# Optimization experiments

Hardware: AMD Instinct MI355X
Metric: run time of the kernel (lower is better)

## Reference

```python
import jax, jax.numpy as jnp
import numpy as np

EPS = 1e-6

def layernorm(x, alpha, bias):
    # torch.std default is unbiased (ddof=1)
    mean = x.mean(axis=-1, keepdims=True)
    std = jnp.std(x, axis=-1, keepdims=True, ddof=1)
    return alpha * (x - mean) / (std + EPS) + bias


def setup_inputs() -> dict:
    key = jax.random.key(0)
    B, L, d_model = 2, 1024, 1024
    d_state, d_conv, expand = 16, 4, 2
    d_inner = expand * d_model
    ks = jax.random.split(key, 8)
    std = 0.02
    x = jax.random.normal(ks[0], (B, L, d_model), dtype=jnp.float32)
    in_proj_w = jax.random.normal(ks[1], (2 * d_inner, d_model), dtype=jnp.float32) * std
    in_proj_b = jnp.zeros((2 * d_inner,), jnp.float32)
    conv_w = jax.random.normal(ks[2], (d_inner, 1, d_conv), dtype=jnp.float32) * std  # depthwise, groups=d_inner
    conv_b = jnp.zeros((d_inner,), jnp.float32)
    x_proj_w = jax.random.normal(ks[3], (2 * d_state, d_inner), dtype=jnp.float32) * std
    x_proj_b = jnp.zeros((2 * d_state,), jnp.float32)
    dt_proj_w = jax.random.normal(ks[4], (d_inner, d_inner), dtype=jnp.float32) * std
    dt_proj_b = jnp.zeros((d_inner,), jnp.float32)
    A_log = jnp.log(jnp.tile(jnp.arange(1, d_state + 1, dtype=jnp.float32), (d_inner, 1)))
    D = jnp.ones((d_inner,), jnp.float32)
    out_proj_w = jax.random.normal(ks[5], (d_model, d_inner), dtype=jnp.float32) * std
    out_proj_b = jnp.zeros((d_model,), jnp.float32)
    in_norm_alpha = jnp.ones((d_model,), jnp.float32)
    in_norm_bias = jnp.zeros((d_model,), jnp.float32)
    norm_alpha = jnp.ones((d_model,), jnp.float32)
    norm_bias = jnp.zeros((d_model,), jnp.float32)
    return {"x": x, "in_proj_w": in_proj_w, "in_proj_b": in_proj_b,
            "conv_w": conv_w, "conv_b": conv_b,
            "x_proj_w": x_proj_w, "x_proj_b": x_proj_b,
            "dt_proj_w": dt_proj_w, "dt_proj_b": dt_proj_b,
            "A_log": A_log, "D": D,
            "out_proj_w": out_proj_w, "out_proj_b": out_proj_b,
            "in_norm_alpha": in_norm_alpha, "in_norm_bias": in_norm_bias,
            "norm_alpha": norm_alpha, "norm_bias": norm_bias}


def reference(x, in_proj_w, in_proj_b, conv_w, conv_b, x_proj_w, x_proj_b,
              dt_proj_w, dt_proj_b, A_log, D, out_proj_w, out_proj_b,
              in_norm_alpha, in_norm_bias, norm_alpha, norm_bias):
    batch, L, d_model = x.shape
    d_inner = D.shape[0]
    d_state = A_log.shape[1]
    d_conv = conv_w.shape[-1]

    residual = x
    xn = layernorm(x, in_norm_alpha, in_norm_bias)
    xz = xn @ in_proj_w.T + in_proj_b                    # (B, L, 2*d_inner)
    x_in, z = jnp.split(xz, 2, axis=-1)

    # causal depthwise conv: torch pads both sides by d_conv-1 then slices [:L]
    # -> equivalent to left-pad only
    xc = jnp.swapaxes(x_in, 1, 2)                        # (B, d_inner, L)
    xc = jax.lax.conv_general_dilated(
        xc, conv_w, window_strides=(1,), padding=[(d_conv - 1, 0)],
        dimension_numbers=('NCH', 'OIH', 'NCH'),
        feature_group_count=d_inner) + conv_b[None, :, None]
    xc = jax.nn.silu(jnp.swapaxes(xc, 1, 2))             # (B, L, d_inner)

    Bmat, Cmat = jnp.split(xc @ x_proj_w.T + x_proj_b, 2, axis=-1)  # (B, L, d_state) each
    delta = jnp.clip(jax.nn.softplus(xc @ dt_proj_w.T + dt_proj_b), 1e-4, 10.0)
    A = -jnp.exp(A_log)                                  # (d_inner, d_state)
    flags = (jnp.arange(L) % 16) == 15                   # periodic renorm mask

    def step(h, inp):
        d_t, B_t, C_t, x_t, flag = inp                   # d_t,x_t: (B,d_inner); B_t,C_t: (B,d_state)
        dA = jnp.exp(jnp.clip(d_t[..., None] * A, -10.0, 0.0))      # (B,d_inner,d_state)
        dBx = d_t[..., None] * B_t[:, None, :] * x_t[..., None]
        h = dA * h + dBx
        hn = jnp.maximum(jnp.linalg.norm(h, axis=-1, keepdims=True), 1e-6)
        scale = jnp.where(hn > 10.0, 10.0 / hn, 1.0)
        h = jnp.where(flag, h * scale, h)
        y_t = jnp.sum(C_t[:, None, :] * h, axis=-1) + D * x_t
        return h, y_t

    h0 = jnp.zeros((batch, d_inner, d_state), dtype=x.dtype)
    xs = (jnp.swapaxes(delta, 0, 1), jnp.swapaxes(Bmat, 0, 1),
          jnp.swapaxes(Cmat, 0, 1), jnp.swapaxes(xc, 0, 1), flags)
    _, ys = jax.lax.scan(step, h0, xs)                   # ys: (L, B, d_inner)
    y = jnp.swapaxes(ys, 0, 1)

    y = y * jax.nn.silu(z)
    out = y @ out_proj_w.T + out_proj_b                  # dropout is identity in eval
    return layernorm(residual + out, norm_alpha, norm_bias)
```

## Files before the change

kernel.cpp:

```cpp
#include <hip/hip_runtime.h>
#include <math.h>

typedef unsigned short u16;
typedef unsigned int   u32;
typedef __bf16 bf16x8 __attribute__((ext_vector_type(8)));
typedef float  f32x4  __attribute__((ext_vector_type(4)));
typedef u16    u16x8  __attribute__((ext_vector_type(8)));

#define NB   2
#define LL   1024
#define DM   1024
#define DI   2048
#define MM   (NB*LL)
#define NXZ  (2*DI)
#define DSTATE 16
#define NSEG 64
#define NDT  2176
#define F32PAT 0x3F800000u

__device__ __forceinline__ float b2f(u16 u) {
  union { u32 i; float f; } v; v.i = ((u32)u) << 16; return v.f;
}
__device__ __forceinline__ u16 f2b(float f) {
  union { float f; u32 i; } v; v.f = f;
  u32 r = (v.i + 0x7FFFu + ((v.i >> 16) & 1u)) >> 16;
  return (u16)r;
}
__device__ __forceinline__ float ldx(const void* p, size_t i, bool isf32) {
  return isf32 ? ((const float*)p)[i] : b2f(((const u16*)p)[i]);
}

typedef __attribute__((address_space(1))) const void gas_t;
typedef __attribute__((address_space(3))) void las_t;
__device__ __forceinline__ void gload_lds16(const void* g, void* l) {
  __builtin_amdgcn_global_load_lds((gas_t*)g, (las_t*)l, 16, 0, 0);
}

__global__ __launch_bounds__(256) void ln1_kernel(
    const void* __restrict__ x, const void* __restrict__ alpha,
    const void* __restrict__ beta, u16* __restrict__ out,
    const u32* __restrict__ probe)
{
  const bool isf32 = (*probe == F32PAT);
  int row = blockIdx.x;
  int base = threadIdx.x * 4;
  size_t ix = (size_t)row * DM + base;
  float v0, v1, v2, v3;
  if (isf32) {
    float4 f = *(const float4*)((const float*)x + ix);
    v0 = f.x; v1 = f.y; v2 = f.z; v3 = f.w;
  } else {
    ushort4 u = *(const ushort4*)((const u16*)x + ix);
    v0 = b2f(u.x); v1 = b2f(u.y); v2 = b2f(u.z); v3 = b2f(u.w);
  }
  float s  = v0 + v1 + v2 + v3;
  float ss = v0*v0 + v1*v1 + v2*v2 + v3*v3;
#pragma unroll
  for (int off = 32; off > 0; off >>= 1) {
    s  += __shfl_down(s,  off);
    ss += __shfl_down(ss, off);
  }
  __shared__ float sb[4], ssb[4];
  int wv = threadIdx.x >> 6, ln = threadIdx.x & 63;
  if (ln == 0) { sb[wv] = s; ssb[wv] = ss; }
  __syncthreads();
  s  = sb[0]  + sb[1]  + sb[2]  + sb[3];
  ss = ssb[0] + ssb[1] + ssb[2] + ssb[3];
  float mean = s * (1.0f / DM);
  float var  = fmaxf((ss - (float)DM * mean * mean) * (1.0f / (DM - 1)), 0.0f);
  float inv  = 1.0f / (sqrtf(var) + 1e-6f);
  float a0 = ldx(alpha, base+0, isf32), a1 = ldx(alpha, base+1, isf32);
  float a2 = ldx(alpha, base+2, isf32), a3 = ldx(alpha, base+3, isf32);
  float b0 = ldx(beta,  base+0, isf32), b1 = ldx(beta,  base+1, isf32);
  float b2 = ldx(beta,  base+2, isf32), b3 = ldx(beta,  base+3, isf32);
  ushort4 o;
  o.x = f2b(a0 * (v0 - mean) * inv + b0);
  o.y = f2b(a1 * (v1 - mean) * inv + b1);
  o.z = f2b(a2 * (v2 - mean) * inv + b2);
  o.w = f2b(a3 * (v3 - mean) * inv + b3);
  *(ushort4*)(out + ix) = o;
}

__global__ __launch_bounds__(256) void ln2_kernel(
    const void* __restrict__ x, const float* __restrict__ outp,
    const void* __restrict__ alpha, const void* __restrict__ beta,
    void* __restrict__ out, const u32* __restrict__ probe)
{
  const bool isf32 = (*probe == F32PAT);
  int row = blockIdx.x;
  int base = threadIdx.x * 4;
  size_t ix = (size_t)row * DM + base;
  float v0, v1, v2, v3;
  if (isf32) {
    float4 f = *(const float4*)((const float*)x + ix);
    v0 = f.x; v1 = f.y; v2 = f.z; v3 = f.w;
  } else {
    ushort4 u = *(const ushort4*)((const u16*)x + ix);
    v0 = b2f(u.x); v1 = b2f(u.y); v2 = b2f(u.z); v3 = b2f(u.w);
  }
  float4 p = *(const float4*)(outp + ix);
  v0 += p.x; v1 += p.y; v2 += p.z; v3 += p.w;
  float s  = v0 + v1 + v2 + v3;
  float ss = v0*v0 + v1*v1 + v2*v2 + v3*v3;
#pragma unroll
  for (int off = 32; off > 0; off >>= 1) {
    s  += __shfl_down(s,  off);
    ss += __shfl_down(ss, off);
  }
  __shared__ float sb[4], ssb[4];
  int wv = threadIdx.x >> 6, ln = threadIdx.x & 63;
  if (ln == 0) { sb[wv] = s; ssb[wv] = ss; }
  __syncthreads();
  s  = sb[0]  + sb[1]  + sb[2]  + sb[3];
  ss = ssb[0] + ssb[1] + ssb[2] + ssb[3];
  float mean = s * (1.0f / DM);
  float var  = fmaxf((ss - (float)DM * mean * mean) * (1.0f / (DM - 1)), 0.0f);
  float inv  = 1.0f / (sqrtf(var) + 1e-6f);
  float a0 = ldx(alpha, base+0, isf32), a1 = ldx(alpha, base+1, isf32);
  float a2 = ldx(alpha, base+2, isf32), a3 = ldx(alpha, base+3, isf32);
  float b0 = ldx(beta,  base+0, isf32), b1 = ldx(beta,  base+1, isf32);
  float b2 = ldx(beta,  base+2, isf32), b3 = ldx(beta,  base+3, isf32);
  float r0 = a0 * (v0 - mean) * inv + b0;
  float r1 = a1 * (v1 - mean) * inv + b1;
  float r2 = a2 * (v2 - mean) * inv + b2;
  float r3 = a3 * (v3 - mean) * inv + b3;
  if (isf32) {
    float4 o; o.x = r0; o.y = r1; o.z = r2; o.w = r3;
    *(float4*)((float*)out + ix) = o;
  } else {
    ushort4 o; o.x = f2b(r0); o.y = f2b(r1); o.z = f2b(r2); o.w = f2b(r3);
    *(ushort4*)((u16*)out + ix) = o;
  }
}

__global__ __launch_bounds__(256) void ln2_sk_kernel(
    const void* __restrict__ x, const float* __restrict__ P,
    const void* __restrict__ op_bias,
    const void* __restrict__ alpha, const void* __restrict__ beta,
    void* __restrict__ out, const u32* __restrict__ probe)
{
  const bool isf32 = (*probe == F32PAT);
  int row = blockIdx.x;
  int base = threadIdx.x * 4;
  size_t ix = (size_t)row * DM + base;
  float v0, v1, v2, v3;
  if (isf32) {
    float4 f = *(const float4*)((const float*)x + ix);
    v0 = f.x; v1 = f.y; v2 = f.z; v3 = f.w;
  } else {
    ushort4 u = *(const ushort4*)((const u16*)x + ix);
    v0 = b2f(u.x); v1 = b2f(u.y); v2 = b2f(u.z); v3 = b2f(u.w);
  }
  v0 += ldx(op_bias, base+0, isf32);
  v1 += ldx(op_bias, base+1, isf32);
  v2 += ldx(op_bias, base+2, isf32);
  v3 += ldx(op_bias, base+3, isf32);
#pragma unroll
  for (int sk = 0; sk < 4; ++sk) {
    float4 p = *(const float4*)(P + ((size_t)sk * MM + row) * DM + base);
    v0 += p.x; v1 += p.y; v2 += p.z; v3 += p.w;
  }
  float s  = v0 + v1 + v2 + v3;
  float ss = v0*v0 + v1*v1 + v2*v2 + v3*v3;
#pragma unroll
  for (int off = 32; off > 0; off >>= 1) {
    s  += __shfl_down(s,  off);
    ss += __shfl_down(ss, off);
  }
  __shared__ float sb[4], ssb[4];
  int wv = threadIdx.x >> 6, ln = threadIdx.x & 63;
  if (ln == 0) { sb[wv] = s; ssb[wv] = ss; }
  __syncthreads();
  s  = sb[0]  + sb[1]  + sb[2]  + sb[3];
  ss = ssb[0] + ssb[1] + ssb[2] + ssb[3];
  float mean = s * (1.0f / DM);
  float var  = fmaxf((ss - (float)DM * mean * mean) * (1.0f / (DM - 1)), 0.0f);
  float inv  = 1.0f / (sqrtf(var) + 1e-6f);
  float a0 = ldx(alpha, base+0, isf32), a1 = ldx(alpha, base+1, isf32);
  float a2 = ldx(alpha, base+2, isf32), a3 = ldx(alpha, base+3, isf32);
  float b0 = ldx(beta,  base+0, isf32), b1 = ldx(beta,  base+1, isf32);
  float b2 = ldx(beta,  base+2, isf32), b3 = ldx(beta,  base+3, isf32);
  float r0 = a0 * (v0 - mean) * inv + b0;
  float r1 = a1 * (v1 - mean) * inv + b1;
  float r2 = a2 * (v2 - mean) * inv + b2;
  float r3 = a3 * (v3 - mean) * inv + b3;
  if (isf32) {
    float4 o; o.x = r0; o.y = r1; o.z = r2; o.w = r3;
    *(float4*)((float*)out + ix) = o;
  } else {
    ushort4 o; o.x = f2b(r0); o.y = f2b(r1); o.z = f2b(r2); o.w = f2b(r3);
    *(ushort4*)((u16*)out + ix) = o;
  }
}

#define CVT_A  4194304u
#define CVT_B  8388608u
#define CVT_C 10485760u
#define CVT_D 10551296u
#define CVT_E 10747904u

__global__ __launch_bounds__(256) void cvt_kernel(
    const void* __restrict__ s_in, const void* __restrict__ s_dt,
    const void* __restrict__ s_op, const void* __restrict__ s_xp,
    u16* __restrict__ inpw, u16* __restrict__ wdt, u16* __restrict__ opw,
    const u32* __restrict__ probe)
{
  const bool isf32 = (*probe == F32PAT);
  size_t i4 = ((size_t)blockIdx.x * 256 + threadIdx.x) * 4;
  if (i4 >= CVT_E) return;
  const void* src; u16* dst; size_t off;
  if      (i4 < CVT_A) { src = s_in; dst = inpw;        off = i4; }
  else if (i4 < CVT_B) { src = s_dt; dst = wdt;         off = i4 - CVT_A; }
  else if (i4 < CVT_C) { src = s_op; dst = opw;         off = i4 - CVT_B; }
  else if (i4 < CVT_D) { src = s_xp; dst = wdt + CVT_A; off = i4 - CVT_C; }
  else {
    ushort4 z = {0, 0, 0, 0};
    *(ushort4*)(wdt + 4259840u + (i4 - CVT_D)) = z;
    return;
  }
  ushort4 o;
  if (isf32) {
    float4 f = *(const float4*)((const float*)src + off);
    o.x = f2b(f.x); o.y = f2b(f.y); o.z = f2b(f.z); o.w = f2b(f.w);
  } else {
    o = *(const ushort4*)((const u16*)src + off);
  }
  *(ushort4*)(dst + off) = o;
}

__device__ __forceinline__ void stage64(const u16* __restrict__ G, int rowK,
                                        int k0, u16* __restrict__ lds,
                                        int wave, int lane, int m0) {
#pragma unroll
  for (int q = 0; q < 4; ++q) {
    int ci = (wave * 4 + q) * 64 + lane;
    int r  = ci >> 3;
    int s  = ci & 7;
    int ch = s ^ (r & 7);
    const u16* ga = G + (size_t)(m0 + r) * rowK + k0 + ch * 8;
    gload_lds16(ga, lds + (size_t)ci * 8);
  }
}
__device__ __forceinline__ bf16x8 frag64(const u16* __restrict__ lds,
                                         int r, int ch) {
  int s = ch ^ (r & 7);
  return *(const bf16x8*)(lds + (size_t)r * 64 + s * 8);
}

#define EPI_NONE 0
#define EPI_SOFTPLUS 1

template<int EPI, int OUTBF>
__global__ __launch_bounds__(256) void gemm_fast(
    const u16* __restrict__ A, const u16* __restrict__ W,
    const void* __restrict__ bias, void* __restrict__ Cout,
    const u32* __restrict__ probe, int M, int N, int K)
{
  __shared__ __align__(16) u16 As[128 * 64];
  __shared__ __align__(16) u16 Ws[128 * 64];
  const bool isf32 = (*probe == F32PAT);
  const int tid  = threadIdx.x;
  const int wave = tid >> 6;
  const int lane = tid & 63;
  const int quad = lane >> 4;
  const int l16  = lane & 15;
  const int m0 = blockIdx.x * 128;
  const int n0 = blockIdx.y * 128;
  const int wm = (wave >> 1) * 64;
  const int wn = (wave & 1) * 64;

  f32x4 acc[4][4] = {};

  for (int k0 = 0; k0 < K; k0 += 64) {
    __syncthreads();
    stage64(A, K, k0, As, wave, lane, m0);
    stage64(W, K, k0, Ws, wave, lane, n0);
    __syncthreads();
#pragma unroll
    for (int kk = 0; kk < 2; ++kk) {
      bf16x8 af[4], bfr[4];
#pragma unroll
      for (int i = 0; i < 4; ++i) {
        af[i]  = frag64(As, wm + i * 16 + l16, kk * 4 + quad);
        bfr[i] = frag64(Ws, wn + i * 16 + l16, kk * 4 + quad);
      }
#pragma unroll
      for (int i = 0; i < 4; ++i)
#pragma unroll
        for (int j = 0; j < 4; ++j)
          acc[i][j] = __builtin_amdgcn_mfma_f32_16x16x32_bf16(af[i], bfr[j], acc[i][j], 0, 0, 0);
    }
  }

#pragma unroll
  for (int i = 0; i < 4; ++i) {
    int rbase = m0 + wm + i * 16 + quad * 4;
#pragma unroll
    for (int j = 0; j < 4; ++j) {
      int col = n0 + wn + j * 16 + l16;
      float bv = ldx(bias, col, isf32);
#pragma unroll
      for (int r = 0; r < 4; ++r) {
        float v = acc[i][j][r] + bv;
        if (EPI == EPI_SOFTPLUS) {
          v = (v > 20.0f) ? v : __logf(1.0f + __expf(v));
          v = fminf(fmaxf(v, 1e-4f), 10.0f);
        }
        size_t oi = (size_t)(rbase + r) * N + col;
        if (OUTBF) ((u16*)Cout)[oi] = f2b(v);
        else       ((float*)Cout)[oi] = v;
      }
    }
  }
}

__global__ __launch_bounds__(256) void gemm_sk(
    const u16* __restrict__ A, const u16* __restrict__ W,
    float* __restrict__ P, int M, int N, int Kfull, int Kslice)
{
  __shared__ __align__(16) u16 As[128 * 64];
  __shared__ __align__(16) u16 Ws[128 * 64];
  const int tid  = threadIdx.x;
  const int wave = tid >> 6;
  const int lane = tid & 63;
  const int quad = lane >> 4;
  const int l16  = lane & 15;
  const int m0 = blockIdx.x * 128;
  const int n0 = blockIdx.y * 128;
  const int sk = blockIdx.z;
  const int kbeg = sk * Kslice;
  const int kend = kbeg + Kslice;
  const int wm = (wave >> 1) * 64;
  const int wn = (wave & 1) * 64;

  f32x4 acc[4][4] = {};

  for (int k0 = kbeg; k0 < kend; k0 += 64) {
    __syncthreads();
    stage64(A, Kfull, k0, As, wave, lane, m0);
    stage64(W, Kfull, k0, Ws, wave, lane, n0);
    __syncthreads();
#pragma unroll
    for (int kk = 0; kk < 2; ++kk) {
      bf16x8 af[4], bfr[4];
#pragma unroll
      for (int i = 0; i < 4; ++i) {
        af[i]  = frag64(As, wm + i * 16 + l16, kk * 4 + quad);
        bfr[i] = frag64(Ws, wn + i * 16 + l16, kk * 4 + quad);
      }
#pragma unroll
      for (int i = 0; i < 4; ++i)
#pragma unroll
        for (int j = 0; j < 4; ++j)
          acc[i][j] = __builtin_amdgcn_mfma_f32_16x16x32_bf16(af[i], bfr[j], acc[i][j], 0, 0, 0);
    }
  }

  float* Pb = P + (size_t)sk * M * N;
#pragma unroll
  for (int i = 0; i < 4; ++i) {
    int rbase = m0 + wm + i * 16 + quad * 4;
#pragma unroll
    for (int j = 0; j < 4; ++j) {
      int col = n0 + wn + j * 16 + l16;
#pragma unroll
      for (int r = 0; r < 4; ++r)
        Pb[(size_t)(rbase + r) * N + col] = acc[i][j][r];
    }
  }
}

__global__ __launch_bounds__(256) void reduce_combo(
    const float* __restrict__ P, const void* __restrict__ bias_dt,
    const void* __restrict__ bias_xp, float* __restrict__ delta,
    float* __restrict__ bc, const u32* __restrict__ probe)
{
  const bool isf32 = (*probe == F32PAT);
  const int m = blockIdx.x;
  const float* p0 = P + (size_t)m * NDT;
  const float* p1 = P + (size_t)(MM + m) * NDT;
  for (int n = threadIdx.x; n < DI + 32; n += 256) {
    float v = p0[n] + p1[n];
    if (n < DI) {
      v += ldx(bias_dt, n, isf32);
      v = (v > 20.0f) ? v : __logf(1.0f + __expf(v));
      v = fminf(fmaxf(v, 1e-4f), 10.0f);
      delta[(size_t)m * DI + n] = v;
    } else {
      bc[(size_t)m * 32 + (n - DI)] = v + ldx(bias_xp, n - DI, isf32);
    }
  }
}

template<int EPI, int OUTBF>
__global__ __launch_bounds__(256) void gemm_r2(
    const u16* __restrict__ A, const void* __restrict__ W,
    const void* __restrict__ bias, void* __restrict__ Cout,
    const u32* __restrict__ probe, int M, int N, int K)
{
  __shared__ __align__(16) u16 As[128 * 32];
  __shared__ __align__(16) u16 Ws[128 * 32];
  const bool isf32 = (*probe == F32PAT);
  const int tid  = threadIdx.x;
  const int wave = tid >> 6;
  const int lane = tid & 63;
  const int quad = lane >> 4;
  const int l16  = lane & 15;
  const int m0 = blockIdx.x * 128;
  const int n0 = blockIdx.y * 128;
  const int wm = (wave >> 1) * 64;
  const int wn = (wave & 1) * 64;

  f32x4 acc[4][4] = {};

  for (int k0 = 0; k0 < K; k0 += 32) {
    u16x8 va[2], vw[2];
#pragma unroll
    for (int q = 0; q < 2; ++q) {
      int ci  = wave * 128 + q * 64 + lane;
      int row = ci >> 2;
      int kc  = (ci & 3) * 8;
      va[q] = *(const u16x8*)(A + (size_t)(m0 + row) * K + k0 + kc);
      size_t wi = (size_t)(n0 + row) * K + k0 + kc;
      if (isf32) {
        const float* Wf = (const float*)W;
        float4 f0 = *(const float4*)(Wf + wi);
        float4 f1 = *(const float4*)(Wf + wi + 4);
        u16x8 t;
        t[0] = f2b(f0.x); t[1] = f2b(f0.y); t[2] = f2b(f0.z); t[3] = f2b(f0.w);
        t[4] = f2b(f1.x); t[5] = f2b(f1.y); t[6] = f2b(f1.z); t[7] = f2b(f1.w);
        vw[q] = t;
      } else {
        vw[q] = *(const u16x8*)((const u16*)W + wi);
      }
    }
    __syncthreads();
#pragma unroll
    for (int q = 0; q < 2; ++q) {
      int ci = wave * 128 + q * 64 + lane;
      *(u16x8*)(As + (size_t)ci * 8) = va[q];
      *(u16x8*)(Ws + (size_t)ci * 8) = vw[q];
    }
    __syncthreads();
    bf16x8 af[4], bfr[4];
#pragma unroll
    for (int i = 0; i < 4; ++i) {
      af[i]  = *(const bf16x8*)(As + (size_t)(wm + i * 16 + l16) * 32 + quad * 8);
      bfr[i] = *(const bf16x8*)(Ws + (size_t)(wn + i * 16 + l16) * 32 + quad * 8);
    }
#pragma unroll
    for (int i = 0; i < 4; ++i)
#pragma unroll
      for (int j = 0; j < 4; ++j)
        acc[i][j] = __builtin_amdgcn_mfma_f32_16x16x32_bf16(af[i], bfr[j], acc[i][j], 0, 0, 0);
  }

#pragma unroll
  for (int i = 0; i < 4; ++i) {
    int rbase = m0 + wm + i * 16 + quad * 4;
#pragma unroll
    for (int j = 0; j < 4; ++j) {
      int col = n0 + wn + j * 16 + l16;
      float bv = ldx(bias, col, isf32);
#pragma unroll
      for (int r = 0; r < 4; ++r) {
        float v = acc[i][j][r] + bv;
        if (EPI == EPI_SOFTPLUS) {
          v = (v > 20.0f) ? v : __logf(1.0f + __expf(v));
          v = fminf(fmaxf(v, 1e-4f), 10.0f);
        }
        size_t oi = (size_t)(rbase + r) * N + col;
        if (OUTBF) ((u16*)Cout)[oi] = f2b(v);
        else       ((float*)Cout)[oi] = v;
      }
    }
  }
}

__global__ __launch_bounds__(256) void conv_silu_kernel(
    const u16* __restrict__ xz, const void* __restrict__ cw,
    const void* __restrict__ cb, u16* __restrict__ xc_bf,
    const u32* __restrict__ probe)
{
  const bool isf32 = (*probe == F32PAT);
  int g = blockIdx.x * 256 + threadIdx.x;
  int c = g & (DI - 1);
  int m = g >> 11;
  int l = m & (LL - 1);
  float w0 = ldx(cw, c*4+0, isf32), w1 = ldx(cw, c*4+1, isf32);
  float w2 = ldx(cw, c*4+2, isf32), w3 = ldx(cw, c*4+3, isf32);
  const u16* col = xz + (size_t)m * NXZ + c;
  float acc = ldx(cb, c, isf32);
  acc += w3 * b2f(col[0]);
  if (l >= 1) acc += w2 * b2f(*(col - NXZ));
  if (l >= 2) acc += w1 * b2f(*(col - 2*NXZ));
  if (l >= 3) acc += w0 * b2f(*(col - 3*NXZ));
  float sil = acc / (1.0f + __expf(-acc));
  xc_bf[g] = f2b(sil);
}

__global__ __launch_bounds__(256) void proj_bc_r2(
    const u16* __restrict__ xc, const void* __restrict__ W,
    const void* __restrict__ bias, float* __restrict__ bc,
    const u32* __restrict__ probe)
{
  const bool isf32 = (*probe == F32PAT);
  int m = blockIdx.x;
  int n = threadIdx.x >> 3;
  int part = threadIdx.x & 7;
  const u16* xr = xc + (size_t)m * DI + part * 256;
  size_t wbase = (size_t)n * DI + part * 256;
  float acc = 0.0f;
  if (isf32) {
    const float* wr = (const float*)W + wbase;
#pragma unroll 8
    for (int i = 0; i < 256; i += 4) {
      ushort4 xv = *(const ushort4*)(xr + i);
      float4  wv = *(const float4*)(wr + i);
      acc += b2f(xv.x)*wv.x + b2f(xv.y)*wv.y + b2f(xv.z)*wv.z + b2f(xv.w)*wv.w;
    }
  } else {
    const u16* wr = (const u16*)W + wbase;
#pragma unroll 8
    for (int i = 0; i < 256; i += 4) {
      ushort4 xv = *(const ushort4*)(xr + i);
      ushort4 wv = *(const ushort4*)(wr + i);
      acc += b2f(xv.x)*b2f(wv.x) + b2f(xv.y)*b2f(wv.y)
           + b2f(xv.z)*b2f(wv.z) + b2f(xv.w)*b2f(wv.w);
    }
  }
  __shared__ float ps[256];
  ps[threadIdx.x] = acc;
  __syncthreads();
  if (threadIdx.x < 32) {
    float s = 0.0f;
#pragma unroll
    for (int p = 0; p < 8; ++p) s += ps[threadIdx.x * 8 + p];
    bc[(size_t)m * 32 + threadIdx.x] = s + ldx(bias, threadIdx.x, isf32);
  }
}

__global__ __launch_bounds__(256, 4) void scan_p1(
    const float* __restrict__ delta, const float* __restrict__ bc,
    const u16* __restrict__ xc, const void* __restrict__ A_log,
    float2* __restrict__ PQ, const u32* __restrict__ probe)
{
  const bool isf32 = (*probe == F32PAT);
  const int c = blockIdx.x * 256 + threadIdx.x;
  const int g = blockIdx.y;
  const int b = blockIdx.z;
  const int row0 = b * LL + g * 16;
  __shared__ float sBC[512];
  if (threadIdx.x < 128)
    *(float4*)&sBC[threadIdx.x * 4] =
        *(const float4*)(bc + (size_t)row0 * 32 + threadIdx.x * 4);
  float Av2[16];
#pragma unroll
  for (int s = 0; s < 16; ++s)
    Av2[s] = -__expf(ldx(A_log, (size_t)c * DSTATE + s, isf32)) * 1.44269504f;
  float p[16], q[16];
#pragma unroll
  for (int s = 0; s < 16; ++s) { p[s] = 1.0f; q[s] = 0.0f; }
  __syncthreads();
  const float CLIP2 = -14.4269504f;
#pragma unroll 4
  for (int j = 0; j < 16; ++j) {
    int row = row0 + j;
    float d  = delta[(size_t)row * DI + c];
    float x  = b2f(xc[(size_t)row * DI + c]);
    float dx = d * x;
    float4 B4[4];
    B4[0] = *(const float4*)&sBC[j * 32 + 0];
    B4[1] = *(const float4*)&sBC[j * 32 + 4];
    B4[2] = *(const float4*)&sBC[j * 32 + 8];
    B4[3] = *(const float4*)&sBC[j * 32 + 12];
    const float* Bv = (const float*)B4;
#pragma unroll
    for (int s = 0; s < 16; ++s) {
      float a = __builtin_amdgcn_exp2f(fmaxf(d * Av2[s], CLIP2));
      q[s] = a * q[s] + dx * Bv[s];
      p[s] *= a;
    }
  }
  float2* out = PQ + ((size_t)(b * NSEG + g) * DI + c) * DSTATE;
#pragma unroll
  for (int s = 0; s < 16; ++s) out[s] = make_float2(p[s], q[s]);
}

__global__ __launch_bounds__(256) void scan_p2(
    const float2* __restrict__ PQ, float* __restrict__ Hin,
    float* __restrict__ Scale)
{
  const int s = threadIdx.x & 15;
  const int c = blockIdx.x * 16 + (threadIdx.x >> 4);
  const int b = blockIdx.y;
  const size_t stride = (size_t)DI * DSTATE;
  const size_t base = ((size_t)b * NSEG * DI + c) * DSTATE + s;
  float h = 0.0f;
  float2 pq = PQ[base];
  for (int g = 0; g < NSEG; ++g) {
    float2 cur = pq;
    if (g < NSEG - 1) pq = PQ[base + (size_t)(g + 1) * stride];
    Hin[base + (size_t)g * stride] = h;
    h = cur.x * h + cur.y;
    float n2 = h * h;
    n2 += __shfl_xor(n2, 1);
    n2 += __shfl_xor(n2, 2);
    n2 += __shfl_xor(n2, 4);
    n2 += __shfl_xor(n2, 8);
    float hn = fmaxf(sqrtf(n2), 1e-6f);
    float sc = hn > 10.0f ? 10.0f / hn : 1.0f;
    if (s == 0) Scale[((size_t)b * NSEG + g) * DI + c] = sc;
    h *= sc;
  }
}

__global__ __launch_bounds__(256, 4) void scan_p3(
    const float* __restrict__ delta, const float* __restrict__ bc,
    const u16* __restrict__ xc, const u16* __restrict__ xz,
    const void* __restrict__ A_log, const void* __restrict__ Dp,
    const float* __restrict__ Hin, const float* __restrict__ Scale,
    u16* __restrict__ y_bf, const u32* __restrict__ probe)
{
  const bool isf32 = (*probe == F32PAT);
  const int c = blockIdx.x * 256 + threadIdx.x;
  const int g = blockIdx.y;
  const int b = blockIdx.z;
  const int row0 = b * LL + g * 16;
  __shared__ float sBC[512];
  if (threadIdx.x < 128)
    *(float4*)&sBC[threadIdx.x * 4] =
        *(const float4*)(bc + (size_t)row0 * 32 + threadIdx.x * 4);
  float Av2[16];
#pragma unroll
  for (int s = 0; s < 16; ++s)
    Av2[s] = -__expf(ldx(A_log, (size_t)c * DSTATE + s, isf32)) * 1.44269504f;
  float h[16];
  const float* hp = Hin + ((size_t)(b * NSEG + g) * DI + c) * DSTATE;
#pragma unroll
  for (int s4 = 0; s4 < 4; ++s4)
    *(float4*)&h[s4 * 4] = *(const float4*)(hp + s4 * 4);
  const float sc15 = Scale[((size_t)b * NSEG + g) * DI + c];
  const float Dc = ldx(Dp, c, isf32);
  __syncthreads();
  const float CLIP2 = -14.4269504f;
#pragma unroll 4
  for (int j = 0; j < 16; ++j) {
    int row = row0 + j;
    float d  = delta[(size_t)row * DI + c];
    float x  = b2f(xc[(size_t)row * DI + c]);
    float z  = b2f(xz[(size_t)row * NXZ + DI + c]);
    float dx = d * x;
    float4 BC[8];
    BC[0] = *(const float4*)&sBC[j * 32 + 0];
    BC[1] = *(const float4*)&sBC[j * 32 + 4];
    BC[2] = *(const float4*)&sBC[j * 32 + 8];
    BC[3] = *(const float4*)&sBC[j * 32 + 12];
    BC[4] = *(const float4*)&sBC[j * 32 + 16];
    BC[5] = *(const float4*)&sBC[j * 32 + 20];
    BC[6] = *(const float4*)&sBC[j * 32 + 24];
    BC[7] = *(const float4*)&sBC[j * 32 + 28];
    const float* Bv = (const float*)BC;
    const float* Cv = Bv + 16;
#pragma unroll
    for (int s = 0; s < 16; ++s) {
      float a = __builtin_amdgcn_exp2f(fmaxf(d * Av2[s], CLIP2));
      h[s] = a * h[s] + dx * Bv[s];
    }
    if (j == 15) {
#pragma unroll
      for (int s = 0; s < 16; ++s) h[s] *= sc15;
    }
    float ys = 0.0f;
#pragma unroll
    for (int s = 0; s < 16; ++s) ys += Cv[s] * h[s];
    float yo = (ys + Dc * x) * (z / (1.0f + __expf(-z)));
    y_bf[(size_t)row * DI + c] = f2b(yo);
  }
}

__global__ __launch_bounds__(256) void scan_mono(
    const float* __restrict__ delta, const float* __restrict__ bc,
    const u16* __restrict__ xc, const u16* __restrict__ xz,
    const void* __restrict__ A_log, const void* __restrict__ Dp,
    u16* __restrict__ y_bf, const u32* __restrict__ probe)
{
  const bool isf32 = (*probe == F32PAT);
  const int s = threadIdx.x & 15;
  const int c = blockIdx.x * 16 + (threadIdx.x >> 4);
  const int b = blockIdx.y;
  const float Av2 = -__expf(ldx(A_log, (size_t)c * DSTATE + s, isf32)) * 1.44269504f;
  const float Dc  = ldx(Dp, c, isf32);
  const float CLIP2 = -14.4269504f;
  float h = 0.0f;
  for (int t0 = 0; t0 < LL; t0 += 16) {
    float dl[16], xl[16], zl[16], Bv[16], Cv[16];
#pragma unroll
    for (int j = 0; j < 16; ++j) {
      int row = b * LL + t0 + j;
      dl[j] = delta[(size_t)row * DI + c];
      xl[j] = b2f(xc[(size_t)row * DI + c]);
      zl[j] = b2f(xz[(size_t)row * NXZ + DI + c]);
      Bv[j] = bc[(size_t)row * 32 + s];
      Cv[j] = bc[(size_t)row * 32 + 16 + s];
    }
#pragma unroll
    for (int j = 0; j < 16; ++j) {
      float d = dl[j], x = xl[j];
      float dA = __builtin_amdgcn_exp2f(fmaxf(d * Av2, CLIP2));
      h = dA * h + (d * x) * Bv[j];
      if (j == 15) {
        float n2 = h * h;
        n2 += __shfl_xor(n2, 1); n2 += __shfl_xor(n2, 2);
        n2 += __shfl_xor(n2, 4); n2 += __shfl_xor(n2, 8);
        float hn = fmaxf(sqrtf(n2), 1e-6f);
        float sc = hn > 10.0f ? 10.0f / hn : 1.0f;
        h *= sc;
      }
      float ys = Cv[j] * h;
      ys += __shfl_xor(ys, 1); ys += __shfl_xor(ys, 2);
      ys += __shfl_xor(ys, 4); ys += __shfl_xor(ys, 8);
      float z = zl[j];
      float yo = (ys + Dc * x) * (z / (1.0f + __expf(-z)));
      if (s == 0) {
        int row = b * LL + t0 + j;
        y_bf[(size_t)row * DI + c] = f2b(yo);
      }
    }
  }
}

extern "C" void kernel_launch(void* const* d_in, const int* in_sizes, int n_in,
                              void* d_out, int out_size, void* d_ws, size_t ws_size,
                              hipStream_t stream) {
  const void* x          = d_in[0];
  const void* in_proj_w  = d_in[1];
  const void* in_proj_b  = d_in[2];
  const void* conv_w     = d_in[3];
  const void* conv_b     = d_in[4];
  const void* x_proj_w   = d_in[5];
  const void* x_proj_b   = d_in[6];
  const void* dt_proj_w  = d_in[7];
  const void* dt_proj_b  = d_in[8];
  const void* A_log      = d_in[9];
  const void* Dp         = d_in[10];
  const void* out_proj_w = d_in[11];
  const void* out_proj_b = d_in[12];
  const void* in_norm_a  = d_in[13];
  const void* in_norm_b  = d_in[14];
  const void* norm_a     = d_in[15];
  const void* norm_b     = d_in[16];
  const u32*  probe      = (const u32*)d_in[13];

  const size_t MiB = 1048576;
  const size_t NEED_NEW = 106299392;

  if (ws_size >= NEED_NEW) {
    char* w = (char*)d_ws;
    u16*   xz_bf = (u16*)w;    w += 16 * MiB;
    u16*   xc_bf = (u16*)w;    w += 8 * MiB;
    float* delta = (float*)w;  w += 16 * MiB;
    float* bc    = (float*)w;  w += 256 * 1024;
    float* Scale = (float*)w;  w += 1 * MiB;
    u16*   opw   = (u16*)w;    w += 4 * MiB;
    u16*   y_bf  = (u16*)w;    w += 8 * MiB;
    char* S = w;
    u16*    wdt    = (u16*)(S);
    u16*    inpw   = (u16*)(S + 8*MiB + 512*1024);
    u16*    xn_bf  = (u16*)(S + 16*MiB + 512*1024);
    float*  deltaP = (float*)(S + 8*MiB + 512*1024);
    float2* PQ     = (float2*)(S);
    float*  Hin    = (float*)(S + 32*MiB);
    float*  outP   = (float*)(S);

    cvt_kernel<<<10496, 256, 0, stream>>>(in_proj_w, dt_proj_w, out_proj_w, x_proj_w,
                                          inpw, wdt, opw, probe);
    ln1_kernel<<<MM, 256, 0, stream>>>(x, in_norm_a, in_norm_b, xn_bf, probe);
    gemm_fast<EPI_NONE, 1><<<dim3(MM/128, NXZ/128), 256, 0, stream>>>(
        xn_bf, inpw, in_proj_b, xz_bf, probe, MM, NXZ, DM);
    conv_silu_kernel<<<(MM * DI) / 256, 256, 0, stream>>>(xz_bf, conv_w, conv_b, xc_bf, probe);
    gemm_sk<<<dim3(MM/128, NDT/128, 2), 256, 0, stream>>>(
        xc_bf, wdt, deltaP, MM, NDT, DI, DI/2);
    reduce_combo<<<MM, 256, 0, stream>>>(deltaP, dt_proj_b, x_proj_b, delta, bc, probe);
    scan_p1<<<dim3(DI/256, NSEG, NB), 256, 0, stream>>>(delta, bc, xc_bf, A_log, PQ, probe);
    scan_p2<<<dim3(DI/16, NB), 256, 0, stream>>>(PQ, Hin, Scale);
    scan_p3<<<dim3(DI/256, NSEG, NB), 256, 0, stream>>>(
        delta, bc, xc_bf, xz_bf, A_log, Dp, Hin, Scale, y_bf, probe);
    gemm_sk<<<dim3(MM/128, DM/128, 4), 256, 0, stream>>>(
        y_bf, opw, outP, MM, DM, DI, DI/4);
    ln2_sk_kernel<<<MM, 256, 0, stream>>>(x, outP, out_proj_b, norm_a, norm_b, d_out, probe);
  } else {
    char* w = (char*)d_ws;
    u16*   xn_bf = (u16*)w;   w += (size_t)MM * DM * 2;
    u16*   xz_bf = (u16*)w;   w += (size_t)MM * NXZ * 2;
    u16*   xc_bf = (u16*)w;   w += (size_t)MM * DI * 2;
    float* delta = (float*)w; w += (size_t)MM * DI * 4;
    float* bc    = (float*)w; w += (size_t)MM * 32 * 4;
    u16*   y_bf  = (u16*)w;   w += (size_t)MM * DI * 2;
    float* outp  = (float*)w; w += (size_t)MM * DM * 4;

    ln1_kernel<<<MM, 256, 0, stream>>>(x, in_norm_a, in_norm_b, xn_bf, probe);
    gemm_r2<EPI_NONE, 1><<<dim3(MM/128, NXZ/128), 256, 0, stream>>>(
        xn_bf, in_proj_w, in_proj_b, xz_bf, probe, MM, NXZ, DM);
    conv_silu_kernel<<<(MM * DI) / 256, 256, 0, stream>>>(xz_bf, conv_w, conv_b, xc_bf, probe);
    gemm_r2<EPI_SOFTPLUS, 0><<<dim3(MM/128, DI/128), 256, 0, stream>>>(
        xc_bf, dt_proj_w, dt_proj_b, delta, probe, MM, DI, DI);
    proj_bc_r2<<<MM, 256, 0, stream>>>(xc_bf, x_proj_w, x_proj_b, bc, probe);
    scan_mono<<<dim3(DI/16, NB), 256, 0, stream>>>(delta, bc, xc_bf, xz_bf, A_log, Dp, y_bf, probe);
    gemm_r2<EPI_NONE, 0><<<dim3(MM/128, DM/128), 256, 0, stream>>>(
        y_bf, out_proj_w, out_proj_b, outp, probe, MM, DM, DI);
    ln2_kernel<<<MM, 256, 0, stream>>>(x, outp, norm_a, norm_b, d_out, probe);
  }
}
```

Baseline: 340.8 us.

## Fuse split-K reduce into scan passes, bf16 partials, merge cvt and ln1

Drops the reduce_combo kernel: gemm_sk writes its two split-K partials as bf16, and scan_p1/scan_p3 each sum them, add the bias and apply softplus/clip inline when reading delta and B/C. The weight conversion and input layernorm are merged into one launch, and the scan carry Hin is stored as bf16. This removes a full fp32 delta round-trip through memory and two kernel launches. In exchange the softplus is computed twice, once in each scan pass, and bf16 partials and carry lower precision.

```diff
diff --git a/kernel.cpp b/kernel.cpp
--- a/kernel.cpp
+++ b/kernel.cpp
@@ -29,11 +29,92 @@
 __device__ __forceinline__ float ldx(const void* p, size_t i, bool isf32) {
   return isf32 ? ((const float*)p)[i] : b2f(((const u16*)p)[i]);
 }
+__device__ __forceinline__ float spclip(float v) {
+  v = (v > 20.0f) ? v : __logf(1.0f + __expf(v));
+  return fminf(fmaxf(v, 1e-4f), 10.0f);
+}
 
 typedef __attribute__((address_space(1))) const void gas_t;
 typedef __attribute__((address_space(3))) void las_t;
 __device__ __forceinline__ void gload_lds16(const void* g, void* l) {
   __builtin_amdgcn_global_load_lds((gas_t*)g, (las_t*)l, 16, 0, 0);
+}
+
+#define CVT_A  4194304u
+#define CVT_B  8388608u
+#define CVT_C 10485760u
+#define CVT_D 10551296u
+#define CVT_E 10747904u
+#define CVT_BLOCKS 10496
+
+__global__ __launch_bounds__(256) void cvtln_kernel(
+    const void* __restrict__ s_in, const void* __restrict__ s_dt,
+    const void* __restrict__ s_op, const void* __restrict__ s_xp,
+    u16* __restrict__ inpw, u16* __restrict__ wdt, u16* __restrict__ opw,
+    const void* __restrict__ x, const void* __restrict__ alpha,
+    const void* __restrict__ beta, u16* __restrict__ xn,
+    const u32* __restrict__ probe)
+{
+  const bool isf32 = (*probe == F32PAT);
+  __shared__ float sb[4], ssb[4];
+  if (blockIdx.x < CVT_BLOCKS) {
+    size_t i4 = ((size_t)blockIdx.x * 256 + threadIdx.x) * 4;
+    const void* src; u16* dst; size_t off;
+    if      (i4 < CVT_A) { src = s_in; dst = inpw;        off = i4; }
+    else if (i4 < CVT_B) { src = s_dt; dst = wdt;         off = i4 - CVT_A; }
+    else if (i4 < CVT_C) { src = s_op; dst = opw;         off = i4 - CVT_B; }
+    else if (i4 < CVT_D) { src = s_xp; dst = wdt + CVT_A; off = i4 - CVT_C; }
+    else {
+      ushort4 z = {0, 0, 0, 0};
+      *(ushort4*)(wdt + 4259840u + (i4 - CVT_D)) = z;
+      return;
+    }
+    ushort4 o;
+    if (isf32) {
+      float4 f = *(const float4*)((const float*)src + off);
+      o.x = f2b(f.x); o.y = f2b(f.y); o.z = f2b(f.z); o.w = f2b(f.w);
+    } else {
+      o = *(const ushort4*)((const u16*)src + off);
+    }
+    *(ushort4*)(dst + off) = o;
+    return;
+  }
+  int row = blockIdx.x - CVT_BLOCKS;
+  int base = threadIdx.x * 4;
+  size_t ix = (size_t)row * DM + base;
+  float v0, v1, v2, v3;
+  if (isf32) {
+    float4 f = *(const float4*)((const float*)x + ix);
+    v0 = f.x; v1 = f.y; v2 = f.z; v3 = f.w;
+  } else {
+    ushort4 u = *(const ushort4*)((const u16*)x + ix);
+    v0 = b2f(u.x); v1 = b2f(u.y); v2 = b2f(u.z); v3 = b2f(u.w);
+  }
+  float s  = v0 + v1 + v2 + v3;
+  float ss = v0*v0 + v1*v1 + v2*v2 + v3*v3;
+#pragma unroll
+  for (int off = 32; off > 0; off >>= 1) {
+    s  += __shfl_down(s,  off);
+    ss += __shfl_down(ss, off);
+  }
+  int wv = threadIdx.x >> 6, ln = threadIdx.x & 63;
+  if (ln == 0) { sb[wv] = s; ssb[wv] = ss; }
+  __syncthreads();
+  s  = sb[0]  + sb[1]  + sb[2]  + sb[3];
+  ss = ssb[0] + ssb[1] + ssb[2] + ssb[3];
+  float mean = s * (1.0f / DM);
+  float var  = fmaxf((ss - (float)DM * mean * mean) * (1.0f / (DM - 1)), 0.0f);
+  float inv  = 1.0f / (sqrtf(var) + 1e-6f);
+  float a0 = ldx(alpha, base+0, isf32), a1 = ldx(alpha, base+1, isf32);
+  float a2 = ldx(alpha, base+2, isf32), a3 = ldx(alpha, base+3, isf32);
+  float b0 = ldx(beta,  base+0, isf32), b1 = ldx(beta,  base+1, isf32);
+  float b2 = ldx(beta,  base+2, isf32), b3 = ldx(beta,  base+3, isf32);
+  ushort4 o;
+  o.x = f2b(a0 * (v0 - mean) * inv + b0);
+  o.y = f2b(a1 * (v1 - mean) * inv + b1);
+  o.z = f2b(a2 * (v2 - mean) * inv + b2);
+  o.w = f2b(a3 * (v3 - mean) * inv + b3);
+  *(ushort4*)(xn + ix) = o;
 }
 
 __global__ __launch_bounds__(256) void ln1_kernel(
@@ -193,12 +274,6 @@
   }
 }
 
-#define CVT_A  4194304u
-#define CVT_B  8388608u
-#define CVT_C 10485760u
-#define CVT_D 10551296u
-#define CVT_E 10747904u
-
 __global__ __launch_bounds__(256) void cvt_kernel(
     const void* __restrict__ s_in, const void* __restrict__ s_dt,
     const void* __restrict__ s_op, const void* __restrict__ s_xp,
@@ -302,10 +377,7 @@
 #pragma unroll
       for (int r = 0; r < 4; ++r) {
         float v = acc[i][j][r] + bv;
-        if (EPI == EPI_SOFTPLUS) {
-          v = (v > 20.0f) ? v : __logf(1.0f + __expf(v));
-          v = fminf(fmaxf(v, 1e-4f), 10.0f);
-        }
+        if (EPI == EPI_SOFTPLUS) v = spclip(v);
         size_t oi = (size_t)(rbase + r) * N + col;
         if (OUTBF) ((u16*)Cout)[oi] = f2b(v);
         else       ((float*)Cout)[oi] = v;
@@ -314,9 +386,10 @@
   }
 }
 
+template<int PARTBF>
 __global__ __launch_bounds__(256) void gemm_sk(
     const u16* __restrict__ A, const u16* __restrict__ W,
-    float* __restrict__ P, int M, int N, int Kfull, int Kslice)
+    void* __restrict__ P, int M, int N, int Kfull, int Kslice)
 {
   __shared__ __align__(16) u16 As[128 * 64];
   __shared__ __align__(16) u16 Ws[128 * 64];
@@ -356,7 +429,6 @@
     }
   }
 
-  float* Pb = P + (size_t)sk * M * N;
 #pragma unroll
   for (int i = 0; i < 4; ++i) {
     int rbase = m0 + wm + i * 16 + quad * 4;
@@ -364,30 +436,11 @@
     for (int j = 0; j < 4; ++j) {
       int col = n0 + wn + j * 16 + l16;
 #pragma unroll
-      for (int r = 0; r < 4; ++r)
-        Pb[(size_t)(rbase + r) * N + col] = acc[i][j][r];
-    }
-  }
-}
-
-__global__ __launch_bounds__(256) void reduce_combo(
-    const float* __restrict__ P, const void* __restrict__ bias_dt,
-    const void* __restrict__ bias_xp, float* __restrict__ delta,
-    float* __restrict__ bc, const u32* __restrict__ probe)
-{
-  const bool isf32 = (*probe == F32PAT);
-  const int m = blockIdx.x;
-  const float* p0 = P + (size_t)m * NDT;
-  const float* p1 = P + (size_t)(MM + m) * NDT;
-  for (int n = threadIdx.x; n < DI + 32; n += 256) {
-    float v = p0[n] + p1[n];
-    if (n < DI) {
-      v += ldx(bias_dt, n, isf32);
-      v = (v > 20.0f) ? v : __logf(1.0f + __expf(v));
-      v = fminf(fmaxf(v, 1e-4f), 10.0f);
-      delta[(size_t)m * DI + n] = v;
-    } else {
-      bc[(size_t)m * 32 + (n - DI)] = v + ldx(bias_xp, n - DI, isf32);
+      for (int r = 0; r < 4; ++r) {
+        size_t oi = (size_t)sk * M * N + (size_t)(rbase + r) * N + col;
+        if (PARTBF) ((u16*)P)[oi] = f2b(acc[i][j][r]);
+        else        ((float*)P)[oi] = acc[i][j][r];
+      }
     }
   }
 }
@@ -465,10 +518,7 @@
 #pragma unroll
       for (int r = 0; r < 4; ++r) {
         float v = acc[i][j][r] + bv;
-        if (EPI == EPI_SOFTPLUS) {
-          v = (v > 20.0f) ? v : __logf(1.0f + __expf(v));
-          v = fminf(fmaxf(v, 1e-4f), 10.0f);
-        }
+        if (EPI == EPI_SOFTPLUS) v = spclip(v);
         size_t oi = (size_t)(rbase + r) * N + col;
         if (OUTBF) ((u16*)Cout)[oi] = f2b(v);
         else       ((float*)Cout)[oi] = v;
@@ -541,7 +591,8 @@
 }
 
 __global__ __launch_bounds__(256, 4) void scan_p1(
-    const float* __restrict__ delta, const float* __restrict__ bc,
+    const u16* __restrict__ Pdt, const void* __restrict__ bias_dt,
+    const void* __restrict__ bias_xp,
     const u16* __restrict__ xc, const void* __restrict__ A_log,
     float2* __restrict__ PQ, const u32* __restrict__ probe)
 {
@@ -550,14 +601,22 @@
   const int g = blockIdx.y;
   const int b = blockIdx.z;
   const int row0 = b * LL + g * 16;
+  const u16* P0 = Pdt;
+  const u16* P1 = Pdt + (size_t)MM * NDT;
   __shared__ float sBC[512];
-  if (threadIdx.x < 128)
-    *(float4*)&sBC[threadIdx.x * 4] =
-        *(const float4*)(bc + (size_t)row0 * 32 + threadIdx.x * 4);
+  if (threadIdx.x < 128) {
+    int j = threadIdx.x >> 3, k0 = (threadIdx.x & 7) * 4;
+    size_t base = (size_t)(row0 + j) * NDT + DI + k0;
+#pragma unroll
+    for (int i = 0; i < 4; ++i)
+      sBC[j * 32 + k0 + i] = b2f(P0[base + i]) + b2f(P1[base + i])
+                           + ldx(bias_xp, k0 + i, isf32);
+  }
   float Av2[16];
 #pragma unroll
   for (int s = 0; s < 16; ++s)
     Av2[s] = -__expf(ldx(A_log, (size_t)c * DSTATE + s, isf32)) * 1.44269504f;
+  const float bdt = ldx(bias_dt, c, isf32);
   float p[16], q[16];
 #pragma unroll
   for (int s = 0; s < 16; ++s) { p[s] = 1.0f; q[s] = 0.0f; }
@@ -566,7 +625,8 @@
 #pragma unroll 4
   for (int j = 0; j < 16; ++j) {
     int row = row0 + j;
-    float d  = delta[(size_t)row * DI + c];
+    size_t pi = (size_t)row * NDT + c;
+    float d  = spclip(b2f(P0[pi]) + b2f(P1[pi]) + bdt);
     float x  = b2f(xc[(size_t)row * DI + c]);
     float dx = d * x;
     float4 B4[4];
@@ -588,7 +648,7 @@
 }
 
 __global__ __launch_bounds__(256) void scan_p2(
-    const float2* __restrict__ PQ, float* __restrict__ Hin,
+    const float2* __restrict__ PQ, u16* __restrict__ Hin,
     float* __restrict__ Scale)
 {
   const int s = threadIdx.x & 15;
@@ -601,7 +661,7 @@
   for (int g = 0; g < NSEG; ++g) {
     float2 cur = pq;
     if (g < NSEG - 1) pq = PQ[base + (size_t)(g + 1) * stride];
-    Hin[base + (size_t)g * stride] = h;
+    Hin[base + (size_t)g * stride] = f2b(h);
     h = cur.x * h + cur.y;
     float n2 = h * h;
     n2 += __shfl_xor(n2, 1);
@@ -616,10 +676,11 @@
 }
 
 __global__ __launch_bounds__(256, 4) void scan_p3(
-    const float* __restrict__ delta, const float* __restrict__ bc,
+    const u16* __restrict__ Pdt, const void* __restrict__ bias_dt,
+    const void* __restrict__ bias_xp,
     const u16* __restrict__ xc, const u16* __restrict__ xz,
     const void* __restrict__ A_log, const void* __restrict__ Dp,
-    const float* __restrict__ Hin, const float* __restrict__ Scale,
+    const u16* __restrict__ Hin, const float* __restrict__ Scale,
     u16* __restrict__ y_bf, const u32* __restrict__ probe)
 {
   const bool isf32 = (*probe == F32PAT);
@@ -627,19 +688,30 @@
   const int g = blockIdx.y;
   const int b = blockIdx.z;
   const int row0 = b * LL + g * 16;
+  const u16* P0 = Pdt;
+  const u16* P1 = Pdt + (size_t)MM * NDT;
   __shared__ float sBC[512];
-  if (threadIdx.x < 128)
-    *(float4*)&sBC[threadIdx.x * 4] =
-        *(const float4*)(bc + (size_t)row0 * 32 + threadIdx.x * 4);
+  if (threadIdx.x < 128) {
+    int j = threadIdx.x >> 3, k0 = (threadIdx.x & 7) * 4;
+    size_t base = (size_t)(row0 + j) * NDT + DI + k0;
+#pragma unroll
+    for (int i = 0; i < 4; ++i)
+      sBC[j * 32 + k0 + i] = b2f(P0[base + i]) + b2f(P1[base + i])
+                           + ldx(bias_xp, k0 + i, isf32);
+  }
   float Av2[16];
 #pragma unroll
   for (int s = 0; s < 16; ++s)
     Av2[s] = -__expf(ldx(A_log, (size_t)c * DSTATE + s, isf32)) * 1.44269504f;
+  const float bdt = ldx(bias_dt, c, isf32);
   float h[16];
-  const float* hp = Hin + ((size_t)(b * NSEG + g) * DI + c) * DSTATE;
-#pragma unroll
-  for (int s4 = 0; s4 < 4; ++s4)
-    *(float4*)&h[s4 * 4] = *(const float4*)(hp + s4 * 4);
+  const u16* hp = Hin + ((size_t)(b * NSEG + g) * DI + c) * DSTATE;
+  {
+    u16x8 h0 = *(const u16x8*)(hp);
+    u16x8 h1 = *(const u16x8*)(hp + 8);
+#pragma unroll
+    for (int s = 0; s < 8; ++s) { h[s] = b2f(h0[s]); h[8 + s] = b2f(h1[s]); }
+  }
   const float sc15 = Scale[((size_t)b * NSEG + g) * DI + c];
   const float Dc = ldx(Dp, c, isf32);
   __syncthreads();
@@ -647,7 +719,8 @@
 #pragma unroll 4
   for (int j = 0; j < 16; ++j) {
     int row = row0 + j;
-    float d  = delta[(size_t)row * DI + c];
+    size_t pi = (size_t)row * NDT + c;
+    float d  = spclip(b2f(P0[pi]) + b2f(P1[pi]) + bdt);
     float x  = b2f(xc[(size_t)row * DI + c]);
     float z  = b2f(xz[(size_t)row * NXZ + DI + c]);
     float dx = d * x;
@@ -759,34 +832,32 @@
     char* w = (char*)d_ws;
     u16*   xz_bf = (u16*)w;    w += 16 * MiB;
     u16*   xc_bf = (u16*)w;    w += 8 * MiB;
-    float* delta = (float*)w;  w += 16 * MiB;
-    float* bc    = (float*)w;  w += 256 * 1024;
+    u16*   Pdt   = (u16*)w;    w += 17 * MiB;
     float* Scale = (float*)w;  w += 1 * MiB;
     u16*   opw   = (u16*)w;    w += 4 * MiB;
     u16*   y_bf  = (u16*)w;    w += 8 * MiB;
     char* S = w;
-    u16*    wdt    = (u16*)(S);
-    u16*    inpw   = (u16*)(S + 8*MiB + 512*1024);
+    u16*    inpw   = (u16*)(S);
+    u16*    wdt    = (u16*)(S + 8*MiB);
     u16*    xn_bf  = (u16*)(S + 16*MiB + 512*1024);
-    float*  deltaP = (float*)(S + 8*MiB + 512*1024);
     float2* PQ     = (float2*)(S);
-    float*  Hin    = (float*)(S + 32*MiB);
+    u16*    Hin    = (u16*)(S + 32*MiB);
     float*  outP   = (float*)(S);
 
-    cvt_kernel<<<10496, 256, 0, stream>>>(in_proj_w, dt_proj_w, out_proj_w, x_proj_w,
-                                          inpw, wdt, opw, probe);
-    ln1_kernel<<<MM, 256, 0, stream>>>(x, in_norm_a, in_norm_b, xn_bf, probe);
+    cvtln_kernel<<<CVT_BLOCKS + MM, 256, 0, stream>>>(
+        in_proj_w, dt_proj_w, out_proj_w, x_proj_w, inpw, wdt, opw,
+        x, in_norm_a, in_norm_b, xn_bf, probe);
     gemm_fast<EPI_NONE, 1><<<dim3(MM/128, NXZ/128), 256, 0, stream>>>(
         xn_bf, inpw, in_proj_b, xz_bf, probe, MM, NXZ, DM);
     conv_silu_kernel<<<(MM * DI) / 256, 256, 0, stream>>>(xz_bf, conv_w, conv_b, xc_bf, probe);
-    gemm_sk<<<dim3(MM/128, NDT/128, 2), 256, 0, stream>>>(
-        xc_bf, wdt, deltaP, MM, NDT, DI, DI/2);
-    reduce_combo<<<MM, 256, 0, stream>>>(deltaP, dt_proj_b, x_proj_b, delta, bc, probe);
-    scan_p1<<<dim3(DI/256, NSEG, NB), 256, 0, stream>>>(delta, bc, xc_bf, A_log, PQ, probe);
+    gemm_sk<1><<<dim3(MM/128, NDT/128, 2), 256, 0, stream>>>(
+        xc_bf, wdt, Pdt, MM, NDT, DI, DI/2);
+    scan_p1<<<dim3(DI/256, NSEG, NB), 256, 0, stream>>>(
+        Pdt, dt_proj_b, x_proj_b, xc_bf, A_log, PQ, probe);
     scan_p2<<<dim3(DI/16, NB), 256, 0, stream>>>(PQ, Hin, Scale);
     scan_p3<<<dim3(DI/256, NSEG, NB), 256, 0, stream>>>(
-        delta, bc, xc_bf, xz_bf, A_log, Dp, Hin, Scale, y_bf, probe);
-    gemm_sk<<<dim3(MM/128, DM/128, 4), 256, 0, stream>>>(
+        Pdt, dt_proj_b, x_proj_b, xc_bf, xz_bf, A_log, Dp, Hin, Scale, y_bf, probe);
+    gemm_sk<0><<<dim3(MM/128, DM/128, 4), 256, 0, stream>>>(
         y_bf, opw, outP, MM, DM, DI, DI/4);
     ln2_sk_kernel<<<MM, 256, 0, stream>>>(x, outP, out_proj_b, norm_a, norm_b, d_out, probe);
   } else {
@@ -804,7 +875,7 @@
         xn_bf, in_proj_w, in_proj_b, xz_bf, probe, MM, NXZ, DM);
     conv_silu_kernel<<<(MM * DI) / 256, 256, 0, stream>>>(xz_bf, conv_w, conv_b, xc_bf, probe);
     gemm_r2<EPI_SOFTPLUS, 0><<<dim3(MM/128, DI/128), 256, 0, stream>>>(
-        xc_bf, dt_proj_w, dt_proj_b, delta, probe, MM, DI, DI);
+        xn_bf == 0 ? xc_bf : xc_bf, dt_proj_w, dt_proj_b, delta, probe, MM, DI, DI);
     proj_bc_r2<<<MM, 256, 0, stream>>>(xc_bf, x_proj_w, x_proj_b, bc, probe);
     scan_mono<<<dim3(DI/16, NB), 256, 0, stream>>>(delta, bc, xc_bf, xz_bf, A_log, Dp, y_bf, probe);
     gemm_r2<EPI_NONE, 0><<<dim3(MM/128, DM/128), 256, 0, stream>>>(
```

New measurement: 315.1 us. -7.5%, faster.
